# Performance work log

Hardware: AMD Instinct MI355X
Metric: run time of the kernel (lower is better)

## Reference

```python
import jax, jax.numpy as jnp
import numpy as np

N_NODES = 100000
N_EDGES = 1600000
NFEAT = 128
NHID = 128
NCLASS = 40


def gcn_conv(x, W, b, src, dst, n_nodes):
    """PyG-style GCNConv: x' = D^{-1/2}(A+I)D^{-1/2} (x W) + b."""
    h = x @ W  # [N, out]
    loop = jnp.arange(n_nodes, dtype=src.dtype)
    s = jnp.concatenate([src, loop])  # add self-loops
    d = jnp.concatenate([dst, loop])
    deg = jax.ops.segment_sum(jnp.ones_like(s, dtype=h.dtype), d, num_segments=n_nodes)
    dinv = jnp.where(deg > 0, jax.lax.rsqrt(deg), 0.0)
    norm = dinv[s] * dinv[d]  # [E+N]
    msg = h[s] * norm[:, None]  # gather + scale
    out = jax.ops.segment_sum(msg, d, num_segments=n_nodes)  # scatter-add
    return out + b


def setup_inputs() -> dict:
    key = jax.random.key(0)
    ks = jax.random.split(key, 6)
    x = jax.random.normal(ks[0], (N_NODES, NFEAT), dtype=jnp.float32)
    edge_index = jax.random.randint(ks[1], (2, N_EDGES), 0, N_NODES, dtype=jnp.int64)
    sc1 = 1.0 / np.sqrt(NFEAT)
    sc2 = 1.0 / np.sqrt(NHID)
    W1 = jax.random.normal(ks[2], (NFEAT, NHID), dtype=jnp.float32) * sc1
    b1 = jnp.zeros((NHID,), dtype=jnp.float32)
    Wm = jax.random.normal(ks[3], (NHID, NHID), dtype=jnp.float32) * sc2
    bm = jnp.zeros((NHID,), dtype=jnp.float32)
    W2 = jax.random.normal(ks[4], (NHID, NCLASS), dtype=jnp.float32) * sc2
    b2 = jnp.zeros((NCLASS,), dtype=jnp.float32)
    return {"x": x, "edge_index": edge_index, "W1": W1, "b1": b1,
            "Wm": Wm, "bm": bm, "W2": W2, "b2": b2}


def reference(x, edge_index, W1, b1, Wm, bm, W2, b2):
    # StandGCNX forward, eval mode (dropout = identity)
    src, dst = edge_index[0], edge_index[1]
    n = x.shape[0]
    h = jax.nn.relu(gcn_conv(x, W1, b1, src, dst, n))
    h = jax.nn.relu(gcn_conv(h, Wm, bm, src, dst, n))
    out = gcn_conv(h, W2, b2, src, dst, n)
    return out
```

## Files before the change

### kernel.cpp

```cpp
#include <hip/hip_runtime.h>
#include <hip/hip_bf16.h>

typedef __attribute__((ext_vector_type(8))) short bf16x8;
typedef __attribute__((ext_vector_type(4))) float f32x4;

__device__ __forceinline__ ushort bf16rne(float f) {
    uint u = __float_as_uint(f);
    return (ushort)((u + 0x7fffu + ((u >> 16) & 1u)) >> 16);
}
__device__ __forceinline__ void unpack2(uint p, float& a, float& b) {
    a = __uint_as_float(p << 16);
    b = __uint_as_float(p & 0xffff0000u);
}


__global__ __launch_bounds__(256) void k_bhist(const int* __restrict__ dst,
                                               int* __restrict__ bcnt, int E) {
    __shared__ int hist[512];
    int t = threadIdx.x;
    hist[t] = 0; hist[t + 256] = 0;
    __syncthreads();
    int off = blockIdx.x * 4096;
    int cnt = min(4096, E - off);
    for (int i = t; i < cnt; i += 256) atomicAdd(&hist[dst[off + i] >> 8], 1);
    __syncthreads();
    if (hist[t]) atomicAdd(&bcnt[t], hist[t]);
    if (hist[t + 256]) atomicAdd(&bcnt[t + 256], hist[t + 256]);
}

__global__ void k_bscan(const int* __restrict__ bcnt, int* __restrict__ bbase,
                        int* __restrict__ bcur, int nbuck) {
    __shared__ int s[512];
    int t = threadIdx.x;
    s[t] = (t < nbuck) ? bcnt[t] : 0;
    __syncthreads();
    for (int d = 1; d < 512; d <<= 1) {
        int u = (t >= d) ? s[t - d] : 0;
        __syncthreads();
        if (t >= d) s[t] += u;
        __syncthreads();
    }
    int excl = (t == 0) ? 0 : s[t - 1];
    bbase[t] = excl;
    if (t < nbuck) bcur[t] = excl;
    if (t == 511) bbase[512] = s[511];
}

__global__ __launch_bounds__(256) void k_binpack(const int* __restrict__ src,
                                                 const int* __restrict__ dst,
                                                 int* __restrict__ bcur,
                                                 uint* __restrict__ pairbuf,
                                                 int E, int nbuck) {
    __shared__ int hist[512];
    __shared__ int scn[512];
    __shared__ int cur[512];
    __shared__ int gbase[512];
    __shared__ uint sorted[4096];
    int t = threadIdx.x;
    int off = blockIdx.x * 4096;
    int cnt = min(4096, E - off);

    hist[t] = 0; hist[t + 256] = 0;
    __syncthreads();
    for (int i = t; i < cnt; i += 256) {
        int b = dst[off + i] >> 8;
        atomicAdd(&hist[b], 1);
    }
    __syncthreads();
    scn[t] = hist[t]; scn[t + 256] = hist[t + 256];
    __syncthreads();
    for (int d = 1; d < 256; d <<= 1) {
        int u0 = (t >= d) ? scn[t - d] : 0;
        int u1 = (t >= d) ? scn[256 + t - d] : 0;
        __syncthreads();
        if (t >= d) { scn[t] += u0; scn[256 + t] += u1; }
        __syncthreads();
    }
    int tot0 = scn[255];
    scn[256 + t] += tot0;
    __syncthreads();
    cur[t] = (t == 0) ? 0 : scn[t - 1];
    cur[t + 256] = scn[t + 255];
    if (t < nbuck && hist[t] > 0) gbase[t] = atomicAdd(&bcur[t], hist[t]);
    int t2 = t + 256;
    if (t2 < nbuck && hist[t2] > 0) gbase[t2] = atomicAdd(&bcur[t2], hist[t2]);
    __syncthreads();
    for (int i = t; i < cnt; i += 256) {
        int d = dst[off + i];
        int s = src[off + i];
        int b = d >> 8;
        int pos = atomicAdd(&cur[b], 1);
        sorted[pos] = ((uint)(d & 255) << 24) | (uint)s;
    }
    __syncthreads();
    int wid = t >> 6, lane = t & 63;
    for (int b = wid; b < nbuck; b += 4) {
        int n = hist[b];
        if (n == 0) continue;
        int ls = (b == 0) ? 0 : scn[b - 1];
        int gb = gbase[b];
        for (int j = lane; j < n; j += 64)
            pairbuf[gb + j] = sorted[ls + j];
    }
}

#define CSR_CAP 5632
__global__ __launch_bounds__(256) void k_csrbuild(const uint* __restrict__ pairbuf,
                                                  const int* __restrict__ bbase,
                                                  int* __restrict__ rowptr,
                                                  float* __restrict__ dinv,
                                                  int* __restrict__ csr,
                                                  int N, int nbuck) {
    __shared__ int lhist[256];
    __shared__ int scn[256];
    __shared__ int lcur[256];
    __shared__ int lcsr[CSR_CAP];
    int b = blockIdx.x;
    int base = b << 8;
    int nn = min(256, N - base);
    int lo = bbase[b], hi = bbase[b + 1];
    int cnt = hi - lo;
    int t = threadIdx.x;
    lhist[t] = 0;
    __syncthreads();
    for (int i = t; i < cnt; i += 256) atomicAdd(&lhist[pairbuf[lo + i] >> 24], 1);
    __syncthreads();
    int mydeg = lhist[t];
    scn[t] = mydeg;
    __syncthreads();
    for (int d = 1; d < 256; d <<= 1) {
        int u = (t >= d) ? scn[t - d] : 0;
        __syncthreads();
        if (t >= d) scn[t] += u;
        __syncthreads();
    }
    int excl = (t == 0) ? 0 : scn[t - 1];
    lcur[t] = excl;
    if (t < nn) {
        rowptr[base + t] = lo + excl;
        dinv[base + t] = rsqrtf((float)(mydeg + 1));
    }
    if (b == nbuck - 1 && t == 0) rowptr[N] = hi;
    __syncthreads();
    if (cnt <= CSR_CAP) {
        for (int i = t; i < cnt; i += 256) {
            uint p = pairbuf[lo + i];
            int pos = atomicAdd(&lcur[p >> 24], 1);
            lcsr[pos] = (int)(p & 0xFFFFFFu);
        }
        __syncthreads();
        for (int i = t; i < cnt; i += 256) csr[lo + i] = lcsr[i];
    } else {
        for (int i = t; i < cnt; i += 256) {
            uint p = pairbuf[lo + i];
            int pos = lo + atomicAdd(&lcur[p >> 24], 1);
            csr[pos] = (int)(p & 0xFFFFFFu);
        }
    }
}


__global__ void k_castT_all(const float* __restrict__ W1, const float* __restrict__ Wm,
                            const float* __restrict__ W2, ushort* __restrict__ w1t,
                            ushort* __restrict__ wmt, ushort* __restrict__ w2t) {
    int b = blockIdx.x;
    int t = threadIdx.x;
    if (b < 64) {
        int i = b * 256 + t; int k = i >> 7, n = i & 127;
        w1t[n * 128 + k] = bf16rne(W1[k * 128 + n]);
    } else if (b < 128) {
        int i = (b - 64) * 256 + t; int k = i >> 7, n = i & 127;
        wmt[n * 128 + k] = bf16rne(Wm[k * 128 + n]);
    } else {
        int i = (b - 128) * 256 + t;
        if (i < 6144) {
            int n = i >> 7, k = i & 127;
            w2t[n * 128 + k] = (n < 40) ? bf16rne(W2[k * 40 + n]) : (ushort)0;
        }
    }
}


__global__ __launch_bounds__(256) void k_gemm1(const float* __restrict__ A,
                                               const ushort* __restrict__ Wt,
                                               const float* __restrict__ dinv,
                                               ushort* __restrict__ C, int M) {
    int t = threadIdx.x;
    int wave = t >> 6, lane = t & 63;
    int m16 = lane & 15, quad = lane >> 4;
    int rowA = blockIdx.x * 64 + wave * 16 + m16;
    int rA = min(rowA, M - 1);
    const float4* A4 = (const float4*)A;

    f32x4 acc[8];
#pragma unroll
    for (int i = 0; i < 8; i++) acc[i] = (f32x4){0.f, 0.f, 0.f, 0.f};

#pragma unroll
    for (int it = 0; it < 4; it++) {
        float4 f0 = A4[(size_t)rA * 32 + 8 * it + 2 * quad];
        float4 f1 = A4[(size_t)rA * 32 + 8 * it + 2 * quad + 1];
        bf16x8 af;
        af[0] = (short)bf16rne(f0.x); af[1] = (short)bf16rne(f0.y);
        af[2] = (short)bf16rne(f0.z); af[3] = (short)bf16rne(f0.w);
        af[4] = (short)bf16rne(f1.x); af[5] = (short)bf16rne(f1.y);
        af[6] = (short)bf16rne(f1.z); af[7] = (short)bf16rne(f1.w);
#pragma unroll
        for (int nt = 0; nt < 8; nt++) {
            bf16x8 bfr = *(const bf16x8*)(Wt + (size_t)(nt * 16 + m16) * 128 + it * 32 + quad * 8);
            acc[nt] = __builtin_amdgcn_mfma_f32_16x16x32_bf16(af, bfr, acc[nt], 0, 0, 0);
        }
    }
    int rowBase = blockIdx.x * 64 + wave * 16 + quad * 4;
    float dnv[4];
#pragma unroll
    for (int r = 0; r < 4; r++) dnv[r] = dinv[min(rowBase + r, M - 1)];
#pragma unroll
    for (int nt = 0; nt < 8; nt++) {
        int col = nt * 16 + m16;
#pragma unroll
        for (int r = 0; r < 4; r++) {
            int row = rowBase + r;
            if (row < M) C[(size_t)row * 128 + col] = bf16rne(acc[nt][r] * dnv[r]);
        }
    }
}


template <int NT>
__device__ __forceinline__ void fused_agg_gemm(const ushort* __restrict__ g,
                                               const float* __restrict__ dinv,
                                               const int* __restrict__ rowptr,
                                               const int* __restrict__ csr,
                                               const float* __restrict__ bias,
                                               const ushort* __restrict__ Wt,
                                               ushort* __restrict__ C,
                                               int M, int ccols) {
    __shared__ ushort hs[64][136];
    int t = threadIdx.x;
    int grp = t >> 4;
    int l = t & 15;
    const uint4* g16 = (const uint4*)g;
    float4 bb0 = ((const float4*)bias)[2 * l];
    float4 bb1 = ((const float4*)bias)[2 * l + 1];

#pragma unroll
    for (int q = 0; q < 4; q++) {
        int node = blockIdx.x * 64 + grp * 4 + q;
        int nd = min(node, M - 1);
        float dn = dinv[nd];
        float a[8];
        {
            uint4 p = g16[(size_t)nd * 16 + l];
            unpack2(p.x, a[0], a[1]); unpack2(p.y, a[2], a[3]);
            unpack2(p.z, a[4], a[5]); unpack2(p.w, a[6], a[7]);
        }
        int e0 = rowptr[nd], e1 = rowptr[nd + 1];
        int e = e0;
        for (; e + 4 <= e1; e += 4) {
            int s0 = csr[e], s1 = csr[e + 1], s2 = csr[e + 2], s3 = csr[e + 3];
            uint4 p0 = g16[(size_t)s0 * 16 + l];
            uint4 p1 = g16[(size_t)s1 * 16 + l];
            uint4 p2 = g16[(size_t)s2 * 16 + l];
            uint4 p3 = g16[(size_t)s3 * 16 + l];
            float u, v;
            unpack2(p0.x, u, v); a[0] += u; a[1] += v;
            unpack2(p0.y, u, v); a[2] += u; a[3] += v;
            unpack2(p0.z, u, v); a[4] += u; a[5] += v;
            unpack2(p0.w, u, v); a[6] += u; a[7] += v;
            unpack2(p1.x, u, v); a[0] += u; a[1] += v;
            unpack2(p1.y, u, v); a[2] += u; a[3] += v;
            unpack2(p1.z, u, v); a[4] += u; a[5] += v;
            unpack2(p1.w, u, v); a[6] += u; a[7] += v;
            unpack2(p2.x, u, v); a[0] += u; a[1] += v;
            unpack2(p2.y, u, v); a[2] += u; a[3] += v;
            unpack2(p2.z, u, v); a[4] += u; a[5] += v;
            unpack2(p2.w, u, v); a[6] += u; a[7] += v;
            unpack2(p3.x, u, v); a[0] += u; a[1] += v;
            unpack2(p3.y, u, v); a[2] += u; a[3] += v;
            unpack2(p3.z, u, v); a[4] += u; a[5] += v;
            unpack2(p3.w, u, v); a[6] += u; a[7] += v;
        }
        for (; e < e1; e++) {
            int s = csr[e];
            uint4 p = g16[(size_t)s * 16 + l];
            float u, v;
            unpack2(p.x, u, v); a[0] += u; a[1] += v;
            unpack2(p.y, u, v); a[2] += u; a[3] += v;
            unpack2(p.z, u, v); a[4] += u; a[5] += v;
            unpack2(p.w, u, v); a[6] += u; a[7] += v;
        }
        float o0 = fmaxf(a[0] * dn + bb0.x, 0.f);
        float o1 = fmaxf(a[1] * dn + bb0.y, 0.f);
        float o2 = fmaxf(a[2] * dn + bb0.z, 0.f);
        float o3 = fmaxf(a[3] * dn + bb0.w, 0.f);
        float o4 = fmaxf(a[4] * dn + bb1.x, 0.f);
        float o5 = fmaxf(a[5] * dn + bb1.y, 0.f);
        float o6 = fmaxf(a[6] * dn + bb1.z, 0.f);
        float o7 = fmaxf(a[7] * dn + bb1.w, 0.f);
        uint4 qv;
        qv.x = (uint)bf16rne(o0) | ((uint)bf16rne(o1) << 16);
        qv.y = (uint)bf16rne(o2) | ((uint)bf16rne(o3) << 16);
        qv.z = (uint)bf16rne(o4) | ((uint)bf16rne(o5) << 16);
        qv.w = (uint)bf16rne(o6) | ((uint)bf16rne(o7) << 16);
        *(uint4*)&hs[grp * 4 + q][l * 8] = qv;
    }
    __syncthreads();

    int wave = t >> 6, lane = t & 63;
    int m16 = lane & 15, quad = lane >> 4;
    f32x4 acc[NT];
#pragma unroll
    for (int i = 0; i < NT; i++) acc[i] = (f32x4){0.f, 0.f, 0.f, 0.f};
#pragma unroll
    for (int it = 0; it < 4; it++) {
        bf16x8 af = *(const bf16x8*)&hs[wave * 16 + m16][it * 32 + quad * 8];
#pragma unroll
        for (int nt = 0; nt < NT; nt++) {
            bf16x8 bfr = *(const bf16x8*)(Wt + (size_t)(nt * 16 + m16) * 128 + it * 32 + quad * 8);
            acc[nt] = __builtin_amdgcn_mfma_f32_16x16x32_bf16(af, bfr, acc[nt], 0, 0, 0);
        }
    }
    int rowBase = blockIdx.x * 64 + wave * 16 + quad * 4;
    float dnv[4];
#pragma unroll
    for (int r = 0; r < 4; r++) dnv[r] = dinv[min(rowBase + r, M - 1)];
#pragma unroll
    for (int nt = 0; nt < NT; nt++) {
        int col = nt * 16 + m16;
        if (col >= ccols) continue;
#pragma unroll
        for (int r = 0; r < 4; r++) {
            int row = rowBase + r;
            if (row < M) C[(size_t)row * ccols + col] = bf16rne(acc[nt][r] * dnv[r]);
        }
    }
}

__global__ __launch_bounds__(256) void k_fusedA(const ushort* __restrict__ g,
                                                const float* __restrict__ dinv,
                                                const int* __restrict__ rowptr,
                                                const int* __restrict__ csr,
                                                const float* __restrict__ bias,
                                                const ushort* __restrict__ Wt,
                                                ushort* __restrict__ C, int M) {
    fused_agg_gemm<8>(g, dinv, rowptr, csr, bias, Wt, C, M, 128);
}

__global__ __launch_bounds__(256) void k_fusedB(const ushort* __restrict__ g,
                                                const float* __restrict__ dinv,
                                                const int* __restrict__ rowptr,
                                                const int* __restrict__ csr,
                                                const float* __restrict__ bias,
                                                const ushort* __restrict__ Wt,
                                                ushort* __restrict__ C, int M) {
    fused_agg_gemm<3>(g, dinv, rowptr, csr, bias, Wt, C, M, 40);
}


__global__ __launch_bounds__(256) void k_agg40_b(const ushort* __restrict__ g3,
                                                 const float* __restrict__ dinv,
                                                 const int* __restrict__ rowptr,
                                                 const int* __restrict__ csr,
                                                 const float* __restrict__ bias,
                                                 float* __restrict__ out, int N) {
    int t = threadIdx.x;
    if (t >= 250) return;
    int grp = t / 10;
    int l = t - grp * 10;
    int node = blockIdx.x * 25 + grp;
    if (node >= N) return;
    const uint2* gp = (const uint2*)g3;
    float dn = dinv[node];
    float a0, a1, a2, a3;
    {
        uint2 p = gp[(size_t)node * 10 + l];
        unpack2(p.x, a0, a1);
        unpack2(p.y, a2, a3);
    }
    int e0 = rowptr[node], e1 = rowptr[node + 1];
    int e = e0;
    for (; e + 4 <= e1; e += 4) {
        int s0 = csr[e], s1 = csr[e + 1], s2 = csr[e + 2], s3 = csr[e + 3];
        uint2 p0 = gp[(size_t)s0 * 10 + l];
        uint2 p1 = gp[(size_t)s1 * 10 + l];
        uint2 p2 = gp[(size_t)s2 * 10 + l];
        uint2 p3 = gp[(size_t)s3 * 10 + l];
        float u, v;
        unpack2(p0.x, u, v); a0 += u; a1 += v;
        unpack2(p0.y, u, v); a2 += u; a3 += v;
        unpack2(p1.x, u, v); a0 += u; a1 += v;
        unpack2(p1.y, u, v); a2 += u; a3 += v;
        unpack2(p2.x, u, v); a0 += u; a1 += v;
        unpack2(p2.y, u, v); a2 += u; a3 += v;
        unpack2(p3.x, u, v); a0 += u; a1 += v;
        unpack2(p3.y, u, v); a2 += u; a3 += v;
    }
    for (; e < e1; e++) {
        int s = csr[e];
        uint2 p = gp[(size_t)s * 10 + l];
        float u, v;
        unpack2(p.x, u, v); a0 += u; a1 += v;
        unpack2(p.y, u, v); a2 += u; a3 += v;
    }
    float4 bb = ((const float4*)bias)[l];
    float4 o;
    o.x = a0 * dn + bb.x;
    o.y = a1 * dn + bb.y;
    o.z = a2 * dn + bb.z;
    o.w = a3 * dn + bb.w;
    ((float4*)out)[(size_t)node * 10 + l] = o;
}


extern "C" void kernel_launch(void* const* d_in, const int* in_sizes, int n_in,
                              void* d_out, int out_size, void* d_ws, size_t ws_size,
                              hipStream_t stream) {
    const float* x  = (const float*)d_in[0];
    const int* eidx = (const int*)d_in[1];
    const float* W1 = (const float*)d_in[2];
    const float* b1 = (const float*)d_in[3];
    const float* Wm = (const float*)d_in[4];
    const float* bm = (const float*)d_in[5];
    const float* W2 = (const float*)d_in[6];
    const float* b2 = (const float*)d_in[7];
    float* out = (float*)d_out;

    int N = in_sizes[0] / 128;
    int E = in_sizes[1] / 2;
    const int* src = eidx;
    const int* dst = eidx + E;
    int nbuck = (N + 255) >> 8;

    char* ws = (char*)d_ws;
    size_t off = 0;
    auto alloc = [&](size_t bytes) -> void* {
        void* p = ws + off;
        off += (bytes + 255) & ~(size_t)255;
        return p;
    };
    float*  dinv    = (float*)alloc((size_t)N * 4);
    int*    rowptr  = (int*)alloc(((size_t)N + 1) * 4);
    int*    csr     = (int*)alloc((size_t)E * 4);
    uint*   pairbuf = (uint*)alloc((size_t)E * 4);
    int*    bcnt    = (int*)alloc(512 * 4);
    int*    bbase   = (int*)alloc(513 * 4);
    int*    bcur    = (int*)alloc(512 * 4);
    ushort* w1t     = (ushort*)alloc(128 * 128 * 2);
    ushort* wmt     = (ushort*)alloc(128 * 128 * 2);
    ushort* w2t     = (ushort*)alloc(48 * 128 * 2);
    ushort* gbuf    = (ushort*)alloc((size_t)N * 128 * 2);
    ushort* gbuf2   = (ushort*)alloc((size_t)N * 128 * 2);
    ushort* g3      = (ushort*)alloc((size_t)N * 40 * 2);

    hipMemsetAsync(bcnt, 0, 512 * 4, stream);
    k_bhist<<<(E + 4095) / 4096, 256, 0, stream>>>(dst, bcnt, E);
    k_bscan<<<1, 512, 0, stream>>>(bcnt, bbase, bcur, nbuck);
    k_binpack<<<(E + 4095) / 4096, 256, 0, stream>>>(src, dst, bcur, pairbuf, E, nbuck);
    k_csrbuild<<<nbuck, 256, 0, stream>>>(pairbuf, bbase, rowptr, dinv, csr, N, nbuck);
    k_castT_all<<<152, 256, 0, stream>>>(W1, Wm, W2, w1t, wmt, w2t);

    int gblk = (N + 63) / 64;
    k_gemm1<<<gblk, 256, 0, stream>>>(x, w1t, dinv, gbuf, N);
    k_fusedA<<<gblk, 256, 0, stream>>>(gbuf, dinv, rowptr, csr, b1, wmt, gbuf2, N);
    k_fusedB<<<gblk, 256, 0, stream>>>(gbuf2, dinv, rowptr, csr, bm, w2t, g3, N);
    k_agg40_b<<<(N + 24) / 25, 256, 0, stream>>>(g3, dinv, rowptr, csr, b2, out, N);
}
```

Baseline: 411.2 us.

## Make fused aggregate-GEMM wave-local with 32-node blocks and no block barrier

Each wave now aggregates its own 8 nodes into a private shared-memory slice and runs its MFMA tile on those rows, so the block-wide __syncthreads is replaced by a block-scope fence. Blocks cover 32 nodes instead of 64, which doubles the grid and lets waves proceed independently instead of waiting for the slowest gather in the block. The cost is that half of each 16-row MFMA tile is zero padding, so GEMM work per useful row doubles and weight loads are repeated across more blocks. Correctness now depends on lanes of one wave seeing each other's LDS writes after only a fence, with no barrier.

```diff
diff --git a/kernel.cpp b/kernel.cpp
--- a/kernel.cpp
+++ b/kernel.cpp
@@ -228,7 +228,7 @@
 
 
 template <int NT>
-__device__ __forceinline__ void fused_agg_gemm(const ushort* __restrict__ g,
+__device__ __forceinline__ void fused_agg_gemm(const ushort* __restrict__ gsrc,
                                                const float* __restrict__ dinv,
                                                const int* __restrict__ rowptr,
                                                const int* __restrict__ csr,
@@ -236,17 +236,19 @@
                                                const ushort* __restrict__ Wt,
                                                ushort* __restrict__ C,
                                                int M, int ccols) {
-    __shared__ ushort hs[64][136];
-    int t = threadIdx.x;
-    int grp = t >> 4;
-    int l = t & 15;
-    const uint4* g16 = (const uint4*)g;
+    __shared__ ushort hs[4][8][136];
+    int t = threadIdx.x;
+    int wave = t >> 6, lane = t & 63;
+    int grp = (lane >> 4) & 3;
+    int l = lane & 15;
+    const uint4* g16 = (const uint4*)gsrc;
     float4 bb0 = ((const float4*)bias)[2 * l];
     float4 bb1 = ((const float4*)bias)[2 * l + 1];
-
-#pragma unroll
-    for (int q = 0; q < 4; q++) {
-        int node = blockIdx.x * 64 + grp * 4 + q;
+    int waveRow0 = blockIdx.x * 32 + wave * 8;
+
+#pragma unroll
+    for (int q = 0; q < 2; q++) {
+        int node = waveRow0 + grp * 2 + q;
         int nd = min(node, M - 1);
         float dn = dinv[nd];
         float a[8];
@@ -303,36 +305,38 @@
         qv.y = (uint)bf16rne(o2) | ((uint)bf16rne(o3) << 16);
         qv.z = (uint)bf16rne(o4) | ((uint)bf16rne(o5) << 16);
         qv.w = (uint)bf16rne(o6) | ((uint)bf16rne(o7) << 16);
-        *(uint4*)&hs[grp * 4 + q][l * 8] = qv;
-    }
-    __syncthreads();
-
-    int wave = t >> 6, lane = t & 63;
+        *(uint4*)&hs[wave][grp * 2 + q][l * 8] = qv;
+    }
+    __threadfence_block();
+
     int m16 = lane & 15, quad = lane >> 4;
     f32x4 acc[NT];
 #pragma unroll
     for (int i = 0; i < NT; i++) acc[i] = (f32x4){0.f, 0.f, 0.f, 0.f};
 #pragma unroll
     for (int it = 0; it < 4; it++) {
-        bf16x8 af = *(const bf16x8*)&hs[wave * 16 + m16][it * 32 + quad * 8];
+        bf16x8 af = {0, 0, 0, 0, 0, 0, 0, 0};
+        if (m16 < 8) af = *(const bf16x8*)&hs[wave][m16][it * 32 + quad * 8];
 #pragma unroll
         for (int nt = 0; nt < NT; nt++) {
             bf16x8 bfr = *(const bf16x8*)(Wt + (size_t)(nt * 16 + m16) * 128 + it * 32 + quad * 8);
             acc[nt] = __builtin_amdgcn_mfma_f32_16x16x32_bf16(af, bfr, acc[nt], 0, 0, 0);
         }
     }
-    int rowBase = blockIdx.x * 64 + wave * 16 + quad * 4;
-    float dnv[4];
-#pragma unroll
-    for (int r = 0; r < 4; r++) dnv[r] = dinv[min(rowBase + r, M - 1)];
-#pragma unroll
-    for (int nt = 0; nt < NT; nt++) {
-        int col = nt * 16 + m16;
-        if (col >= ccols) continue;
-#pragma unroll
-        for (int r = 0; r < 4; r++) {
-            int row = rowBase + r;
-            if (row < M) C[(size_t)row * ccols + col] = bf16rne(acc[nt][r] * dnv[r]);
+    if (quad < 2) {
+        int rowBase = waveRow0 + quad * 4;
+        float dnv[4];
+#pragma unroll
+        for (int r = 0; r < 4; r++) dnv[r] = dinv[min(rowBase + r, M - 1)];
+#pragma unroll
+        for (int nt = 0; nt < NT; nt++) {
+            int col = nt * 16 + m16;
+            if (col >= ccols) continue;
+#pragma unroll
+            for (int r = 0; r < 4; r++) {
+                int row = rowBase + r;
+                if (row < M) C[(size_t)row * ccols + col] = bf16rne(acc[nt][r] * dnv[r]);
+            }
         }
     }
 }
@@ -460,9 +464,10 @@
     k_csrbuild<<<nbuck, 256, 0, stream>>>(pairbuf, bbase, rowptr, dinv, csr, N, nbuck);
     k_castT_all<<<152, 256, 0, stream>>>(W1, Wm, W2, w1t, wmt, w2t);
 
-    int gblk = (N + 63) / 64;
-    k_gemm1<<<gblk, 256, 0, stream>>>(x, w1t, dinv, gbuf, N);
-    k_fusedA<<<gblk, 256, 0, stream>>>(gbuf, dinv, rowptr, csr, b1, wmt, gbuf2, N);
-    k_fusedB<<<gblk, 256, 0, stream>>>(gbuf2, dinv, rowptr, csr, bm, w2t, g3, N);
+    int gblk64 = (N + 63) / 64;
+    int gblk32 = (N + 31) / 32;
+    k_gemm1<<<gblk64, 256, 0, stream>>>(x, w1t, dinv, gbuf, N);
+    k_fusedA<<<gblk32, 256, 0, stream>>>(gbuf, dinv, rowptr, csr, b1, wmt, gbuf2, N);
+    k_fusedB<<<gblk32, 256, 0, stream>>>(gbuf2, dinv, rowptr, csr, bm, w2t, g3, N);
     k_agg40_b<<<(N + 24) / 25, 256, 0, stream>>>(g3, dinv, rowptr, csr, b2, out, N);
 }
```

Measured after the change: 428.8 us. 4.3% more time.
